# Performance work log

Measured on AMD Instinct MI355X. Metric: run time of the kernel, lower is better.

The kernel has to match this reference:

```python
import jax, jax.numpy as jnp
import numpy as np

D = 256; NH = 8; NL = 4; NP = 4; DFF = 2048; HD = D // NH
SHAPES = [(64, 64), (32, 32), (16, 16), (8, 8)]
B = 2; LEN = sum(h * w for h, w in SHAPES)


def setup_inputs() -> dict:
    key = jax.random.key(0)
    ks = jax.random.split(key, 12)
    def w(k, shape, s=0.02):
        return jax.random.normal(k, shape, jnp.float32) * s
    starts = np.cumsum([0] + [h * w for h, w in SHAPES[:-1]])
    return {
        "src": jax.random.normal(ks[0], (B, LEN, D), jnp.float32),
        "pos": jax.random.normal(ks[1], (B, LEN, D), jnp.float32) * 0.1,
        "spatial_shapes": jnp.array(SHAPES, dtype=jnp.int32),
        "level_start_index": jnp.array(starts, dtype=jnp.int32),
        "w_value": w(ks[2], (D, D)), "b_value": jnp.zeros((D,), jnp.float32),
        "w_off": w(ks[3], (D, NH * NL * NP * 2)), "b_off": w(ks[4], (NH * NL * NP * 2,), 0.1),
        "w_attn": w(ks[5], (D, NH * NL * NP)), "b_attn": jnp.zeros((NH * NL * NP,), jnp.float32),
        "w_out": w(ks[6], (D, D)), "b_out": jnp.zeros((D,), jnp.float32),
        "w1": w(ks[7], (D, DFF)), "b1": jnp.zeros((DFF,), jnp.float32),
        "w2": w(ks[8], (DFF, D)), "b2": jnp.zeros((D,), jnp.float32),
        "g1": jnp.ones((D,), jnp.float32), "be1": jnp.zeros((D,), jnp.float32),
        "g2": jnp.ones((D,), jnp.float32), "be2": jnp.zeros((D,), jnp.float32),
    }


def _layer_norm(x, g, b):
    mu = jnp.mean(x, -1, keepdims=True)
    v = jnp.var(x, -1, keepdims=True)
    return (x - mu) * jax.lax.rsqrt(v + 1e-5) * g + b


def _reference_points(shapes):
    # torch.linspace(0.5, H-0.5, H)/H == (arange(H)+0.5)/H
    refs = []
    for H, W in shapes:
        ry = (jnp.arange(H, dtype=jnp.float32) + 0.5) / H
        rx = (jnp.arange(W, dtype=jnp.float32) + 0.5) / W
        yy, xx = jnp.meshgrid(ry, rx, indexing='ij')
        refs.append(jnp.stack([xx.ravel(), yy.ravel()], -1))
    return jnp.concatenate(refs, 0)  # (Len, 2) as (x, y)


def _ms_deform_sample(value, loc, shapes):
    # value: (B, Len, NH, HD); loc: (B, Lq, NH, NL, NP, 2) normalized [0,1]
    # Replicates torch grid_sample(bilinear, padding='zeros', align_corners=False).
    Bn, Lq = loc.shape[0], loc.shape[1]
    P = loc.shape[4]
    start = 0
    outs = []
    for lvl, (H, W) in enumerate(shapes):
        v = value[:, start:start + H * W].transpose(0, 2, 1, 3)  # (B, NH, HW, HD)
        start += H * W
        l = loc[:, :, :, lvl]                      # (B, Lq, NH, P, 2)
        x = l[..., 0] * W - 0.5
        y = l[..., 1] * H - 0.5
        x0 = jnp.floor(x); y0 = jnp.floor(y)
        dx = x - x0; dy = y - y0
        x0i = x0.astype(jnp.int32); y0i = y0.astype(jnp.int32)
        acc = None
        for xi, yi, wgt in ((x0i, y0i, (1 - dx) * (1 - dy)),
                            (x0i + 1, y0i, dx * (1 - dy)),
                            (x0i, y0i + 1, (1 - dx) * dy),
                            (x0i + 1, y0i + 1, dx * dy)):
            valid = ((xi >= 0) & (xi < W) & (yi >= 0) & (yi < H)).astype(value.dtype)
            idx = jnp.clip(yi, 0, H - 1) * W + jnp.clip(xi, 0, W - 1)  # (B, Lq, NH, P)
            idx = idx.transpose(0, 2, 1, 3).reshape(Bn, NH, Lq * P)
            g = jnp.take_along_axis(v, idx[..., None], axis=2).reshape(Bn, NH, Lq, P, HD)
            w = (wgt * valid).transpose(0, 2, 1, 3)[..., None]  # (B, NH, Lq, P, 1)
            acc = g * w if acc is None else acc + g * w
        outs.append(acc)  # (B, NH, Lq, P, HD)
    return jnp.stack(outs, 3)  # (B, NH, Lq, NL, NP, HD)


def _forward(src, pos, w_value, b_value, w_off, b_off, w_attn, b_attn,
             w_out, b_out, w1, b1, w2, b2, g1, be1, g2, be2, shapes):
    Bn, Lq, _ = src.shape
    q = src + pos  # with_pos_embed
    value = (src @ w_value + b_value).reshape(Bn, Lq, NH, HD)
    off = (q @ w_off + b_off).reshape(Bn, Lq, NH, NL, NP, 2)
    attn = jax.nn.softmax((q @ w_attn + b_attn).reshape(Bn, Lq, NH, NL * NP), -1)
    attn = attn.reshape(Bn, Lq, NH, NL, NP)
    ref = _reference_points(shapes)  # (Len, 2)
    normalizer = jnp.array([[w_, h_] for h_, w_ in shapes], jnp.float32)  # (NL, 2) = (W, H)
    loc = ref[None, :, None, None, None, :] + off / normalizer[None, None, None, :, None, :]
    sampled = _ms_deform_sample(value, loc, shapes)  # (B, NH, Lq, NL, NP, HD)
    out = jnp.einsum('bqhlp,bhqlpd->bqhd', attn, sampled).reshape(Bn, Lq, D)
    out = out @ w_out + b_out
    x = _layer_norm(src + out, g1, be1)           # residual + norm1
    ff = jax.nn.relu(x @ w1 + b1) @ w2 + b2       # FFN (dropout=0)
    return _layer_norm(x + ff, g2, be2)           # residual + norm2


def reference(src, pos, spatial_shapes, level_start_index, w_value, b_value,
              w_off, b_off, w_attn, b_attn, w_out, b_out, w1, b1, w2, b2,
              g1, be1, g2, be2):
    shapes = [tuple(int(v) for v in s) for s in np.asarray(spatial_shapes)]
    return _forward(src, pos, w_value, b_value, w_off, b_off, w_attn, b_attn,
                    w_out, b_out, w1, b1, w2, b2, g1, be1, g2, be2, shapes)
```

## Files before the change

### kernel.cpp

```cpp
#include <hip/hip_runtime.h>
#include <math.h>

#define D 256
#define NH 8
#define NL 4
#define NP 4
#define DFF 2048
#define HD 32
#define BB 2
#define LEN 5440
#define MROWS (BB * LEN)

typedef __attribute__((ext_vector_type(8))) short short8;
typedef __attribute__((ext_vector_type(4))) float f32x4;
typedef unsigned int uint32;

__device__ __forceinline__ unsigned short f2bf(float f) {
    uint32 u = __float_as_uint(f);
    u += 0x7FFF + ((u >> 16) & 1);
    return (unsigned short)(u >> 16);
}
__device__ __forceinline__ float bf2f(unsigned short h) {
    return __uint_as_float(((uint32)h) << 16);
}
__device__ __forceinline__ uint32 pack2(float a, float b) {
    return (uint32)f2bf(a) | ((uint32)f2bf(b) << 16);
}

__device__ __forceinline__ void gl16(const unsigned short* g, unsigned short* l) {
    __builtin_amdgcn_global_load_lds(
        (const __attribute__((address_space(1))) unsigned int*)g,
        (__attribute__((address_space(3))) unsigned int*)l, 16, 0, 0);
}

__device__ __forceinline__ void swz85(int b, int ncols, int& row, int& col) {
    const int gsz = ncols << 3;
    const int full = 10 * gsz;
    if (b < full) {
        const int g = b / gsz, idx = b - g * gsz;
        row = (g << 3) + (idx & 7);
        col = idx >> 3;
    } else {
        const int idx = b - full;
        row = 80 + idx % 5;
        col = idx / 5;
    }
}

__global__ void prep_a(const float* __restrict__ w_value, const float* __restrict__ w_off,
                       const float* __restrict__ w_attn,
                       const float* __restrict__ b_value, const float* __restrict__ b_off,
                       const float* __restrict__ b_attn,
                       const float* __restrict__ src, const float* __restrict__ pos,
                       unsigned short* __restrict__ wqvT, float* __restrict__ bqv,
                       unsigned short* __restrict__ s16, unsigned short* __restrict__ q16) {
    __shared__ float tile[32][33];
    const int blk = blockIdx.x;
    const int t = threadIdx.x;
    if (blk < 160) {
        const float* W; unsigned short* WT; int N, tid;
        if (blk < 64)       { W = w_value; WT = wqvT;             N = 256; tid = blk; }
        else if (blk < 128) { W = w_off;   WT = wqvT + 256 * 256; N = 256; tid = blk - 64; }
        else                { W = w_attn;  WT = wqvT + 512 * 256; N = 128; tid = blk - 128; }
        const int K = 256;
        const int ntx = N >> 5;
        const int nb = (tid % ntx) * 32, kb = (tid / ntx) * 32;
        const int tx = t & 31, ty = t >> 5;
#pragma unroll
        for (int i = 0; i < 32; i += 8)
            tile[ty + i][tx] = W[(size_t)(kb + ty + i) * N + nb + tx];
        __syncthreads();
#pragma unroll
        for (int i = 0; i < 32; i += 8)
            WT[(size_t)(nb + ty + i) * K + kb + tx] = f2bf(tile[tx][ty + i]);
    } else if (blk == 160) {
        for (int i = t; i < 640; i += 256)
            bqv[i] = (i < 256) ? b_value[i] : (i < 512 ? b_off[i - 256] : b_attn[i - 512]);
    } else {
        const int tid = blk - 161;
        const size_t base = (size_t)tid * 4096;
        const float4* s4 = (const float4*)src;
        const float4* p4 = (const float4*)pos;
        ushort4* so = (ushort4*)s16;
        ushort4* qo = (ushort4*)q16;
#pragma unroll
        for (int i = 0; i < 16; i++) {
            const size_t gidx = base + (size_t)i * 256 + t;
            float4 a = s4[gidx], p = p4[gidx];
            ushort4 sv, qv;
            sv.x = f2bf(a.x); sv.y = f2bf(a.y); sv.z = f2bf(a.z); sv.w = f2bf(a.w);
            qv.x = f2bf(a.x + p.x); qv.y = f2bf(a.y + p.y);
            qv.z = f2bf(a.z + p.z); qv.w = f2bf(a.w + p.w);
            so[gidx] = sv; qo[gidx] = qv;
        }
    }
}

__global__ __launch_bounds__(256) void ffn1_gemm(
        const unsigned short* __restrict__ A,
        const unsigned short* __restrict__ BT, const float* __restrict__ bias,
        unsigned short* __restrict__ Cv, int N, int K, int lda, int ldb) {
    __shared__ unsigned short smraw[17408];
    auto Ash = (unsigned short (*)[128][32])smraw;
    auto Bsh = (unsigned short (*)[128][32])(smraw + 8192);

    int rowt, colt;
    swz85(blockIdx.x, N >> 7, rowt, colt);
    const int row0 = rowt * 128, col0 = colt * 128;

    const int t = threadIdx.x;
    const int wave = t >> 6, lane = t & 63;
    const int wr = wave >> 1, wc = wave & 1;
    const int lrow = lane & 15, quad = lane >> 4;
    const int sr = lane >> 2, sc = (lane & 3) * 8;

    const unsigned short* Ab = A + (size_t)row0 * lda;
    const unsigned short* Bb = BT + (size_t)col0 * ldb;

    f32x4 acc[4][4];
#pragma unroll
    for (int i = 0; i < 4; i++)
#pragma unroll
        for (int j = 0; j < 4; j++) acc[i][j] = (f32x4){0.f, 0.f, 0.f, 0.f};

    auto stage = [&](int buf, int kb) {
#pragma unroll
        for (int j = 0; j < 2; j++) {
            const int r = wave * 32 + j * 16;
            gl16(Ab + (size_t)(r + sr) * lda + kb + sc, &Ash[buf][r][0]);
            gl16(Bb + (size_t)(r + sr) * ldb + kb + sc, &Bsh[buf][r][0]);
        }
    };

    stage(0, 0);
    int i = 0;
    for (int kb = 0; kb < K; kb += 32, ++i) {
        __syncthreads();
        if (kb + 32 < K) stage((i + 1) & 1, kb + 32);
        const int cf = i & 1;
        short8 af[4], bfr[4];
#pragma unroll
        for (int mt = 0; mt < 4; mt++)
            af[mt] = *(const short8*)&Ash[cf][wr * 64 + mt * 16 + lrow][quad * 8];
#pragma unroll
        for (int nt = 0; nt < 4; nt++)
            bfr[nt] = *(const short8*)&Bsh[cf][wc * 64 + nt * 16 + lrow][quad * 8];
#pragma unroll
        for (int mt = 0; mt < 4; mt++)
#pragma unroll
            for (int nt = 0; nt < 4; nt++)
                acc[mt][nt] = __builtin_amdgcn_mfma_f32_16x16x32_bf16(
                    af[mt], bfr[nt], acc[mt][nt], 0, 0, 0);
    }

    __syncthreads();
    auto bounce = (unsigned short (*)[136])smraw;
#pragma unroll
    for (int nt = 0; nt < 4; nt++) {
        const int cl = wc * 64 + nt * 16 + lrow;
        const float bv = bias[col0 + cl];
#pragma unroll
        for (int mt = 0; mt < 4; mt++) {
            f32x4 a = acc[mt][nt];
#pragma unroll
            for (int r = 0; r < 4; r++)
                bounce[wr * 64 + mt * 16 + quad * 4 + r][cl] = f2bf(fmaxf(a[r] + bv, 0.f));
        }
    }
    __syncthreads();
#pragma unroll
    for (int pass = 0; pass < 8; pass++) {
        const int rl = pass * 16 + (t >> 4), ch = t & 15;
        *(uint4*)&Cv[(size_t)(row0 + rl) * N + col0 + ch * 8] =
            *(const uint4*)&bounce[rl][ch * 8];
    }
}

template <int NZ>
__global__ __launch_bounds__(256) void splitk_gemm(
        const unsigned short* __restrict__ A, const unsigned short* __restrict__ BT,
        unsigned short* __restrict__ part, int KC, int lda, int ldb) {
    __shared__ unsigned short smraw[17408];
    auto Ash = (unsigned short (*)[128][32])smraw;
    auto Bsh = (unsigned short (*)[128][32])(smraw + 8192);

    int rowt, cc;
    swz85(blockIdx.x, 2 * NZ, rowt, cc);
    const int row0 = rowt * 128;
    const int col0 = (cc & 1) * 128;
    const int z = cc >> 1;
    const int koff = z * KC;
    unsigned short* __restrict__ C = part + (size_t)z * MROWS * 256;

    const int t = threadIdx.x;
    const int wave = t >> 6, lane = t & 63;
    const int wr = wave >> 1, wc = wave & 1;
    const int lrow = lane & 15, quad = lane >> 4;
    const int sr = lane >> 2, sc = (lane & 3) * 8;

    const unsigned short* Ab = A + (size_t)row0 * lda + koff;
    const unsigned short* Bb = BT + (size_t)col0 * ldb + koff;

    f32x4 acc[4][4];
#pragma unroll
    for (int i = 0; i < 4; i++)
#pragma unroll
        for (int j = 0; j < 4; j++) acc[i][j] = (f32x4){0.f, 0.f, 0.f, 0.f};

    auto stage = [&](int buf, int kb) {
#pragma unroll
        for (int j = 0; j < 2; j++) {
            const int r = wave * 32 + j * 16;
            gl16(Ab + (size_t)(r + sr) * lda + kb + sc, &Ash[buf][r][0]);
            gl16(Bb + (size_t)(r + sr) * ldb + kb + sc, &Bsh[buf][r][0]);
        }
    };

    stage(0, 0);
    int i = 0;
    for (int kb = 0; kb < KC; kb += 32, ++i) {
        __syncthreads();
        if (kb + 32 < KC) stage((i + 1) & 1, kb + 32);
        const int cf = i & 1;
        short8 af[4], bfr[4];
#pragma unroll
        for (int mt = 0; mt < 4; mt++)
            af[mt] = *(const short8*)&Ash[cf][wr * 64 + mt * 16 + lrow][quad * 8];
#pragma unroll
        for (int nt = 0; nt < 4; nt++)
            bfr[nt] = *(const short8*)&Bsh[cf][wc * 64 + nt * 16 + lrow][quad * 8];
#pragma unroll
        for (int mt = 0; mt < 4; mt++)
#pragma unroll
            for (int nt = 0; nt < 4; nt++)
                acc[mt][nt] = __builtin_amdgcn_mfma_f32_16x16x32_bf16(
                    af[mt], bfr[nt], acc[mt][nt], 0, 0, 0);
    }

    __syncthreads();
    auto bounce = (unsigned short (*)[136])smraw;
#pragma unroll
    for (int nt = 0; nt < 4; nt++) {
        const int cl = wc * 64 + nt * 16 + lrow;
#pragma unroll
        for (int mt = 0; mt < 4; mt++) {
            f32x4 a = acc[mt][nt];
#pragma unroll
            for (int r = 0; r < 4; r++)
                bounce[wr * 64 + mt * 16 + quad * 4 + r][cl] = f2bf(a[r]);
        }
    }
    __syncthreads();
#pragma unroll
    for (int pass = 0; pass < 8; pass++) {
        const int rl = pass * 16 + (t >> 4), ch = t & 15;
        *(uint4*)&C[(size_t)(row0 + rl) * 256 + col0 + ch * 8] =
            *(const uint4*)&bounce[rl][ch * 8];
    }
}

__global__ __launch_bounds__(256) void gemm_ln(
        const unsigned short* __restrict__ A, const unsigned short* __restrict__ BT,
        const float* __restrict__ bias, const float* __restrict__ rsd,
        const float* __restrict__ g, const float* __restrict__ be,
        unsigned short* __restrict__ out16, int K) {
    __shared__ unsigned short Ash[2][32][32];
    __shared__ unsigned short Bsh[2][256][32];
    __shared__ float red1[4][32], red2[4][32];

    const int row0 = blockIdx.x * 32;
    const int t = threadIdx.x;
    const int wave = t >> 6, lane = t & 63;
    const int lrow = lane & 15, quad = lane >> 4;
    const int sr = lane >> 2, sc = (lane & 3) * 8;

    f32x4 acc[2][4];
#pragma unroll
    for (int i = 0; i < 2; i++)
#pragma unroll
        for (int j = 0; j < 4; j++) acc[i][j] = (f32x4){0.f, 0.f, 0.f, 0.f};

    auto stage = [&](int buf, int kb) {
#pragma unroll
        for (int j = 0; j < 4; j++) {
            const int r = wave * 64 + j * 16;
            gl16(BT + (size_t)(r + sr) * K + kb + sc, &Bsh[buf][r][0]);
        }
        if (wave < 2) {
            const int r = wave * 16;
            gl16(A + (size_t)(row0 + r + sr) * K + kb + sc, &Ash[buf][r][0]);
        }
    };

    stage(0, 0);
    int it = 0;
    for (int kb = 0; kb < K; kb += 32, ++it) {
        __syncthreads();
        if (kb + 32 < K) stage((it + 1) & 1, kb + 32);
        const int cf = it & 1;
        short8 af[2], bfr[4];
#pragma unroll
        for (int mt = 0; mt < 2; mt++)
            af[mt] = *(const short8*)&Ash[cf][mt * 16 + lrow][quad * 8];
#pragma unroll
        for (int nt = 0; nt < 4; nt++)
            bfr[nt] = *(const short8*)&Bsh[cf][wave * 64 + nt * 16 + lrow][quad * 8];
#pragma unroll
        for (int mt = 0; mt < 2; mt++)
#pragma unroll
            for (int nt = 0; nt < 4; nt++)
                acc[mt][nt] = __builtin_amdgcn_mfma_f32_16x16x32_bf16(
                    af[mt], bfr[nt], acc[mt][nt], 0, 0, 0);
    }

    float gv[4], bev[4], bv[4];
#pragma unroll
    for (int nt = 0; nt < 4; nt++) {
        const int col = wave * 64 + nt * 16 + lrow;
        bv[nt] = bias[col];
        gv[nt] = g[col];
        bev[nt] = be[col];
    }

    float v[2][4][4];
#pragma unroll
    for (int mt = 0; mt < 2; mt++)
#pragma unroll
        for (int r = 0; r < 4; r++) {
            const int row = row0 + mt * 16 + quad * 4 + r;
#pragma unroll
            for (int nt = 0; nt < 4; nt++) {
                const int col = wave * 64 + nt * 16 + lrow;
                v[mt][nt][r] = acc[mt][nt][r] + bv[nt] + rsd[(size_t)row * 256 + col];
            }
        }

#pragma unroll
    for (int mt = 0; mt < 2; mt++)
#pragma unroll
        for (int r = 0; r < 4; r++) {
            float s1 = v[mt][0][r] + v[mt][1][r] + v[mt][2][r] + v[mt][3][r];
            float s2 = v[mt][0][r] * v[mt][0][r] + v[mt][1][r] * v[mt][1][r] +
                       v[mt][2][r] * v[mt][2][r] + v[mt][3][r] * v[mt][3][r];
#pragma unroll
            for (int o = 1; o < 16; o <<= 1) {
                s1 += __shfl_xor(s1, o, 16);
                s2 += __shfl_xor(s2, o, 16);
            }
            if (lrow == 0) {
                const int rr = mt * 16 + quad * 4 + r;
                red1[wave][rr] = s1;
                red2[wave][rr] = s2;
            }
        }
    __syncthreads();

#pragma unroll
    for (int mt = 0; mt < 2; mt++)
#pragma unroll
        for (int r = 0; r < 4; r++) {
            const int rr = mt * 16 + quad * 4 + r;
            const float su = red1[0][rr] + red1[1][rr] + red1[2][rr] + red1[3][rr];
            const float sq = red2[0][rr] + red2[1][rr] + red2[2][rr] + red2[3][rr];
            const float mean = su * (1.0f / 256.0f);
            const float var = fmaxf(sq * (1.0f / 256.0f) - mean * mean, 0.f);
            const float rstd = rsqrtf(var + 1e-5f);
            const size_t rowoff = (size_t)(row0 + rr) * 256;
#pragma unroll
            for (int nt = 0; nt < 4; nt++) {
                const int col = wave * 64 + nt * 16 + lrow;
                const float o = (v[mt][nt][r] - mean) * rstd * gv[nt] + bev[nt];
                out16[rowoff + col] = f2bf(o);
            }
        }
}

__global__ __launch_bounds__(256) void qv_gemm(
        const unsigned short* __restrict__ s16, const unsigned short* __restrict__ q16,
        const unsigned short* __restrict__ BT, const float* __restrict__ bias,
        unsigned short* __restrict__ val, unsigned short* __restrict__ qout16) {
    __shared__ unsigned short smraw[17408];
    auto Ash = (unsigned short (*)[128][32])smraw;
    auto Bsh = (unsigned short (*)[128][32])(smraw + 8192);

    int rowt, colt;
    swz85(blockIdx.x, 5, rowt, colt);
    const int row0 = rowt * 128, col0 = colt * 128;

    const int t = threadIdx.x;
    const int wave = t >> 6, lane = t & 63;
    const int wr = wave >> 1, wc = wave & 1;
    const int lrow = lane & 15, quad = lane >> 4;
    const int sr = lane >> 2, sc = (lane & 3) * 8;

    const unsigned short* Ab = ((col0 >= 256) ? q16 : s16) + (size_t)row0 * 256;
    const unsigned short* Bb = BT + (size_t)col0 * 256;

    f32x4 acc[4][4];
#pragma unroll
    for (int i = 0; i < 4; i++)
#pragma unroll
        for (int j = 0; j < 4; j++) acc[i][j] = (f32x4){0.f, 0.f, 0.f, 0.f};

    auto stage = [&](int buf, int kb) {
#pragma unroll
        for (int j = 0; j < 2; j++) {
            const int r = wave * 32 + j * 16;
            gl16(Ab + (size_t)(r + sr) * 256 + kb + sc, &Ash[buf][r][0]);
            gl16(Bb + (size_t)(r + sr) * 256 + kb + sc, &Bsh[buf][r][0]);
        }
    };

    stage(0, 0);
    int i = 0;
    for (int kb = 0; kb < 256; kb += 32, ++i) {
        __syncthreads();
        if (kb + 32 < 256) stage((i + 1) & 1, kb + 32);
        const int cf = i & 1;
        short8 af[4], bfr[4];
#pragma unroll
        for (int mt = 0; mt < 4; mt++)
            af[mt] = *(const short8*)&Ash[cf][wr * 64 + mt * 16 + lrow][quad * 8];
#pragma unroll
        for (int nt = 0; nt < 4; nt++)
            bfr[nt] = *(const short8*)&Bsh[cf][wc * 64 + nt * 16 + lrow][quad * 8];
#pragma unroll
        for (int mt = 0; mt < 4; mt++)
#pragma unroll
            for (int nt = 0; nt < 4; nt++)
                acc[mt][nt] = __builtin_amdgcn_mfma_f32_16x16x32_bf16(
                    af[mt], bfr[nt], acc[mt][nt], 0, 0, 0);
    }

    __syncthreads();
    auto bounce = (unsigned short (*)[136])smraw;
#pragma unroll
    for (int nt = 0; nt < 4; nt++) {
        const int cl = wc * 64 + nt * 16 + lrow;
        const float bv = bias[col0 + cl];
#pragma unroll
        for (int mt = 0; mt < 4; mt++) {
            f32x4 a = acc[mt][nt];
#pragma unroll
            for (int r = 0; r < 4; r++)
                bounce[wr * 64 + mt * 16 + quad * 4 + r][cl] = f2bf(a[r] + bv);
        }
    }
    __syncthreads();
    unsigned short* Cp; int ldc, c0;
    if (col0 < 256) { Cp = val;    ldc = 256; c0 = col0; }
    else            { Cp = qout16; ldc = 384; c0 = col0 - 256; }
#pragma unroll
    for (int pass = 0; pass < 8; pass++) {
        const int rl = pass * 16 + (t >> 4), ch = t & 15;
        *(uint4*)&Cp[(size_t)(row0 + rl) * ldc + c0 + ch * 8] =
            *(const uint4*)&bounce[rl][ch * 8];
    }
}

__global__ void sampler(const unsigned short* __restrict__ val,
                        const unsigned short* __restrict__ qout16,
                        unsigned short* __restrict__ out,
                        const float* __restrict__ w_out, const float* __restrict__ w1,
                        const float* __restrict__ w2,
                        unsigned short* __restrict__ woT, unsigned short* __restrict__ w1T,
                        unsigned short* __restrict__ w2T) {
    __shared__ __align__(16) int   sIdx[2][128][4];
    __shared__ __align__(16) float sW[2][128][4];
    __shared__ float tileT[32][33];
    const int t = threadIdx.x;

    if (blockIdx.x >= MROWS / 2) {
        const int bk = (int)blockIdx.x - MROWS / 2;
        const float* W; unsigned short* WT; int K, N, tid;
        if (bk < 64)       { W = w_out; WT = woT;  K = 256;  N = 256;  tid = bk; }
        else if (bk < 576) { W = w1;    WT = w1T;  K = 256;  N = 2048; tid = bk - 64; }
        else               { W = w2;    WT = w2T;  K = 2048; N = 256;  tid = bk - 576; }
        const int ntx = N >> 5;
        const int nb = (tid % ntx) * 32, kb = (tid / ntx) * 32;
        const int tx = t & 31, ty = t >> 5;
#pragma unroll
        for (int i = 0; i < 32; i += 8)
            tileT[ty + i][tx] = W[(size_t)(kb + ty + i) * N + nb + tx];
        __syncthreads();
#pragma unroll
        for (int i = 0; i < 32; i += 8)
            WT[(size_t)(nb + ty + i) * K + kb + tx] = f2bf(tileT[tx][ty + i]);
        return;
    }

    const int sub = t >> 7;
    const int tt = t & 127;
    const int bq = blockIdx.x * 2 + sub;
    const int b = bq / LEN, q = bq % LEN;

    {
        const int h = tt >> 4, p = tt & 15;
        const int l = p >> 2;

        float refx, refy;
        if (q < 4096) {
            int rq = q >> 6, cq = q & 63;
            refx = (cq + 0.5f) * (1.0f / 64.0f);
            refy = (rq + 0.5f) * (1.0f / 64.0f);
        } else if (q < 5120) {
            int qq = q - 4096;
            int rq = qq >> 5, cq = qq & 31;
            refx = (cq + 0.5f) * (1.0f / 32.0f);
            refy = (rq + 0.5f) * (1.0f / 32.0f);
        } else if (q < 5376) {
            int qq = q - 5120;
            int rq = qq >> 4, cq = qq & 15;
            refx = (cq + 0.5f) * (1.0f / 16.0f);
            refy = (rq + 0.5f) * (1.0f / 16.0f);
        } else {
            int qq = q - 5376;
            int rq = qq >> 3, cq = qq & 7;
            refx = (cq + 0.5f) * (1.0f / 8.0f);
            refy = (rq + 0.5f) * (1.0f / 8.0f);
        }

        float lv = bf2f(qout16[(size_t)bq * 384 + 256 + tt]);
        float mx = lv;
#pragma unroll
        for (int o = 1; o < 16; o <<= 1) mx = fmaxf(mx, __shfl_xor(mx, o, 16));
        float e = expf(lv - mx);
        float s = e;
#pragma unroll
        for (int o = 1; o < 16; o <<= 1) s += __shfl_xor(s, o, 16);
        const float aw = e / s;

        const uint32 opair = *(const uint32*)&qout16[(size_t)bq * 384 + h * 32 + p * 2];
        const float ox = bf2f((unsigned short)opair);
        const float oy = bf2f((unsigned short)(opair >> 16));

        const int LST[4] = {0, 4096, 5120, 5376};
        const int WW = 64 >> l;
        const float rw = 1.0f / (float)WW;

        float x = (refx + ox * rw) * (float)WW - 0.5f;
        float y = (refy + oy * rw) * (float)WW - 0.5f;
        float x0f = floorf(x), y0f = floorf(y);
        float dx = x - x0f, dy = y - y0f;
        int x0 = (int)x0f, y0 = (int)y0f;

        const int base = (b * LEN + LST[l]) * 256 + h * 32;
        int xs[2] = {x0, x0 + 1}, ys[2] = {y0, y0 + 1};
        float wx[2] = {1.f - dx, dx}, wy[2] = {1.f - dy, dy};
        int ic[4]; float wc4[4];
#pragma unroll
        for (int cy = 0; cy < 2; cy++)
#pragma unroll
            for (int cx = 0; cx < 2; cx++) {
                int xi = xs[cx], yi = ys[cy];
                bool vld = (xi >= 0) && (xi < WW) && (yi >= 0) && (yi < WW);
                int xc = min(max(xi, 0), WW - 1);
                int yc = min(max(yi, 0), WW - 1);
                ic[cy * 2 + cx] = base + (yc * WW + xc) * 256;
                wc4[cy * 2 + cx] = vld ? wx[cx] * wy[cy] * aw : 0.f;
            }
        *(int4*)&sIdx[sub][tt][0] = make_int4(ic[0], ic[1], ic[2], ic[3]);
        *(float4*)&sW[sub][tt][0] = make_float4(wc4[0], wc4[1], wc4[2], wc4[3]);
    }
    __syncthreads();

    const int h = tt >> 4, dp = tt & 15;
    const unsigned short* vald = val + 2 * dp;
    float acc0 = 0.f, acc1 = 0.f;
#pragma unroll 4
    for (int p = 0; p < 16; p++) {
        const int r = h * 16 + p;
        int4 iv = *(const int4*)&sIdx[sub][r][0];
        float4 wv = *(const float4*)&sW[sub][r][0];
        uint32 u0 = *(const uint32*)(vald + iv.x);
        uint32 u1 = *(const uint32*)(vald + iv.y);
        uint32 u2 = *(const uint32*)(vald + iv.z);
        uint32 u3 = *(const uint32*)(vald + iv.w);
        acc0 += bf2f((unsigned short)u0) * wv.x + bf2f((unsigned short)u1) * wv.y +
                bf2f((unsigned short)u2) * wv.z + bf2f((unsigned short)u3) * wv.w;
        acc1 += bf2f((unsigned short)(u0 >> 16)) * wv.x + bf2f((unsigned short)(u1 >> 16)) * wv.y +
                bf2f((unsigned short)(u2 >> 16)) * wv.z + bf2f((unsigned short)(u3 >> 16)) * wv.w;
    }
    *(uint32*)&out[(size_t)bq * D + h * HD + 2 * dp] = pack2(acc0, acc1);
}

__global__ void add_ln4(const unsigned short* __restrict__ part16,
                        const float* __restrict__ bias,
                        const unsigned short* __restrict__ rsd16,
                        const float* __restrict__ g, const float* __restrict__ be,
                        float* __restrict__ out) {
    const int wave = threadIdx.x >> 6, lane = threadIdx.x & 63;
    const int row = blockIdx.x * 4 + wave;
    const int c0 = lane * 4;
    const size_t i = (size_t)row * 256 + c0;

    float v[4];
    {
        ushort4 r = *(const ushort4*)&rsd16[i];
        float4 bv = *(const float4*)&bias[c0];
        v[0] = bf2f(r.x) + bv.x; v[1] = bf2f(r.y) + bv.y;
        v[2] = bf2f(r.z) + bv.z; v[3] = bf2f(r.w) + bv.w;
    }
#pragma unroll
    for (int z = 0; z < 4; z++) {
        ushort4 p = *(const ushort4*)&part16[(size_t)z * MROWS * 256 + i];
        v[0] += bf2f(p.x); v[1] += bf2f(p.y); v[2] += bf2f(p.z); v[3] += bf2f(p.w);
    }
    float s1 = v[0] + v[1] + v[2] + v[3];
    float s2 = v[0] * v[0] + v[1] * v[1] + v[2] * v[2] + v[3] * v[3];
#pragma unroll
    for (int o = 32; o > 0; o >>= 1) {
        s1 += __shfl_xor(s1, o, 64);
        s2 += __shfl_xor(s2, o, 64);
    }
    const float mean = s1 * (1.0f / 256.0f);
    const float var = fmaxf(s2 * (1.0f / 256.0f) - mean * mean, 0.f);
    const float rstd = rsqrtf(var + 1e-5f);

    float4 gv = *(const float4*)&g[c0];
    float4 bev = *(const float4*)&be[c0];
    float4 o4;
    o4.x = (v[0] - mean) * rstd * gv.x + bev.x;
    o4.y = (v[1] - mean) * rstd * gv.y + bev.y;
    o4.z = (v[2] - mean) * rstd * gv.z + bev.z;
    o4.w = (v[3] - mean) * rstd * gv.w + bev.w;
    *(float4*)&out[i] = o4;
}

extern "C" void kernel_launch(void* const* d_in, const int* in_sizes, int n_in,
                              void* d_out, int out_size, void* d_ws, size_t ws_size,
                              hipStream_t stream) {
    const float* src     = (const float*)d_in[0];
    const float* pos     = (const float*)d_in[1];
    const float* w_value = (const float*)d_in[4];
    const float* b_value = (const float*)d_in[5];
    const float* w_off   = (const float*)d_in[6];
    const float* b_off   = (const float*)d_in[7];
    const float* w_attn  = (const float*)d_in[8];
    const float* b_attn  = (const float*)d_in[9];
    const float* w_out   = (const float*)d_in[10];
    const float* b_out   = (const float*)d_in[11];
    const float* w1      = (const float*)d_in[12];
    const float* b1      = (const float*)d_in[13];
    const float* w2      = (const float*)d_in[14];
    const float* b2      = (const float*)d_in[15];
    const float* g1      = (const float*)d_in[16];
    const float* be1     = (const float*)d_in[17];
    const float* g2      = (const float*)d_in[18];
    const float* be2     = (const float*)d_in[19];
    float* out = (float*)d_out;

    size_t off = 0;
    auto alloc = [&](size_t bytes) -> char* {
        char* p = (char*)d_ws + off;
        off += (bytes + 255) & ~(size_t)255;
        return p;
    };
    unsigned short* wqvT = (unsigned short*)alloc((size_t)640 * 256 * 2);
    unsigned short* woT  = (unsigned short*)alloc(256 * 256 * 2);
    unsigned short* w1T  = (unsigned short*)alloc((size_t)2048 * 256 * 2);
    unsigned short* w2T  = (unsigned short*)alloc((size_t)256 * 2048 * 2);
    float* bqv           = (float*)alloc(640 * 4);

    unsigned short* s16  = (unsigned short*)alloc((size_t)MROWS * 256 * 2);
    unsigned short* q16  = (unsigned short*)alloc((size_t)MROWS * 256 * 2);
    unsigned short* qout = (unsigned short*)alloc((size_t)MROWS * 384 * 2);
    unsigned short* val  = (unsigned short*)alloc((size_t)MROWS * 256 * 2);
    unsigned short* attn = (unsigned short*)alloc((size_t)MROWS * 256 * 2);
    unsigned short* hb   = (unsigned short*)alloc((size_t)MROWS * 2048 * 2);
    unsigned short* xb16 = (unsigned short*)alloc((size_t)MROWS * 256 * 2);
    unsigned short* part = (unsigned short*)alloc((size_t)4 * MROWS * 256 * 2);

    prep_a<<<331, 256, 0, stream>>>(w_value, w_off, w_attn, b_value, b_off, b_attn,
                                    src, pos, wqvT, bqv, s16, q16);

    qv_gemm<<<425, 256, 0, stream>>>(s16, q16, wqvT, bqv, val, qout);
    sampler<<<MROWS / 2 + 1088, 256, 0, stream>>>(val, qout, attn,
                                                  w_out, w1, w2, woT, w1T, w2T);
    gemm_ln<<<340, 256, 0, stream>>>(attn, woT, b_out, src, g1, be1, xb16, 256);

    ffn1_gemm<<<1360, 256, 0, stream>>>(xb16, w1T, b1, hb, 2048, 256, 256, 256);
    splitk_gemm<4><<<680, 256, 0, stream>>>(hb, w2T, part, 512, 2048, 2048);
    add_ln4<<<MROWS / 4, 256, 0, stream>>>(part, b2, xb16, g2, be2, out);
}
```

Before: 201.7 us.

## Fuse src/pos bf16 conversion into QV GEMM and widen sampler per-thread work

The fp32 to bf16 conversion of src and src+pos moves out of prep_a and into the QV GEMM's A-tile staging. The GEMM now loads fp32 rows with register prefetch one stage ahead, adds pos only for the offset/attention columns, packs to bf16 and writes to a padded LDS tile. This removes the s16/q16 intermediate buffers and their write/read traffic, at the cost of reading fp32 A (twice for q columns) and doing conversion work inside the GEMM. Separately, the sampler now handles four queries per block, with each thread gathering four channels via ushort4 instead of two, which halves the block count and widens each gather.

```diff
diff --git a/kernel.cpp b/kernel.cpp
--- a/kernel.cpp
+++ b/kernel.cpp
@@ -51,49 +51,30 @@
                        const float* __restrict__ w_attn,
                        const float* __restrict__ b_value, const float* __restrict__ b_off,
                        const float* __restrict__ b_attn,
-                       const float* __restrict__ src, const float* __restrict__ pos,
-                       unsigned short* __restrict__ wqvT, float* __restrict__ bqv,
-                       unsigned short* __restrict__ s16, unsigned short* __restrict__ q16) {
+                       unsigned short* __restrict__ wqvT, float* __restrict__ bqv) {
     __shared__ float tile[32][33];
     const int blk = blockIdx.x;
     const int t = threadIdx.x;
-    if (blk < 160) {
-        const float* W; unsigned short* WT; int N, tid;
-        if (blk < 64)       { W = w_value; WT = wqvT;             N = 256; tid = blk; }
-        else if (blk < 128) { W = w_off;   WT = wqvT + 256 * 256; N = 256; tid = blk - 64; }
-        else                { W = w_attn;  WT = wqvT + 512 * 256; N = 128; tid = blk - 128; }
-        const int K = 256;
-        const int ntx = N >> 5;
-        const int nb = (tid % ntx) * 32, kb = (tid / ntx) * 32;
-        const int tx = t & 31, ty = t >> 5;
-#pragma unroll
-        for (int i = 0; i < 32; i += 8)
-            tile[ty + i][tx] = W[(size_t)(kb + ty + i) * N + nb + tx];
-        __syncthreads();
-#pragma unroll
-        for (int i = 0; i < 32; i += 8)
-            WT[(size_t)(nb + ty + i) * K + kb + tx] = f2bf(tile[tx][ty + i]);
-    } else if (blk == 160) {
+    if (blk >= 160) {
         for (int i = t; i < 640; i += 256)
             bqv[i] = (i < 256) ? b_value[i] : (i < 512 ? b_off[i - 256] : b_attn[i - 512]);
-    } else {
-        const int tid = blk - 161;
-        const size_t base = (size_t)tid * 4096;
-        const float4* s4 = (const float4*)src;
-        const float4* p4 = (const float4*)pos;
-        ushort4* so = (ushort4*)s16;
-        ushort4* qo = (ushort4*)q16;
-#pragma unroll
-        for (int i = 0; i < 16; i++) {
-            const size_t gidx = base + (size_t)i * 256 + t;
-            float4 a = s4[gidx], p = p4[gidx];
-            ushort4 sv, qv;
-            sv.x = f2bf(a.x); sv.y = f2bf(a.y); sv.z = f2bf(a.z); sv.w = f2bf(a.w);
-            qv.x = f2bf(a.x + p.x); qv.y = f2bf(a.y + p.y);
-            qv.z = f2bf(a.z + p.z); qv.w = f2bf(a.w + p.w);
-            so[gidx] = sv; qo[gidx] = qv;
-        }
-    }
+        return;
+    }
+    const float* W; unsigned short* WT; int N, tid;
+    if (blk < 64)       { W = w_value; WT = wqvT;             N = 256; tid = blk; }
+    else if (blk < 128) { W = w_off;   WT = wqvT + 256 * 256; N = 256; tid = blk - 64; }
+    else                { W = w_attn;  WT = wqvT + 512 * 256; N = 128; tid = blk - 128; }
+    const int K = 256;
+    const int ntx = N >> 5;
+    const int nb = (tid % ntx) * 32, kb = (tid / ntx) * 32;
+    const int tx = t & 31, ty = t >> 5;
+#pragma unroll
+    for (int i = 0; i < 32; i += 8)
+        tile[ty + i][tx] = W[(size_t)(kb + ty + i) * N + nb + tx];
+    __syncthreads();
+#pragma unroll
+    for (int i = 0; i < 32; i += 8)
+        WT[(size_t)(nb + ty + i) * K + kb + tx] = f2bf(tile[tx][ty + i]);
 }
 
 __global__ __launch_bounds__(256) void ffn1_gemm(
@@ -376,24 +357,28 @@
 }
 
 __global__ __launch_bounds__(256) void qv_gemm(
-        const unsigned short* __restrict__ s16, const unsigned short* __restrict__ q16,
+        const float* __restrict__ src, const float* __restrict__ pos,
         const unsigned short* __restrict__ BT, const float* __restrict__ bias,
         unsigned short* __restrict__ val, unsigned short* __restrict__ qout16) {
-    __shared__ unsigned short smraw[17408];
-    auto Ash = (unsigned short (*)[128][32])smraw;
-    auto Bsh = (unsigned short (*)[128][32])(smraw + 8192);
+    __shared__ unsigned short smraw[18432];
+    auto Ash = (unsigned short (*)[128][40])smraw;
+    auto Bsh = (unsigned short (*)[128][32])(smraw + 10240);
 
     int rowt, colt;
     swz85(blockIdx.x, 5, rowt, colt);
     const int row0 = rowt * 128, col0 = colt * 128;
+    const bool addp = (col0 >= 256);
 
     const int t = threadIdx.x;
     const int wave = t >> 6, lane = t & 63;
     const int wr = wave >> 1, wc = wave & 1;
     const int lrow = lane & 15, quad = lane >> 4;
+    const int srow = t >> 1;
+    const int cb = (t & 1) * 16;
     const int sr = lane >> 2, sc = (lane & 3) * 8;
 
-    const unsigned short* Ab = ((col0 >= 256) ? q16 : s16) + (size_t)row0 * 256;
+    const float* ap = src + (size_t)(row0 + srow) * 256 + cb;
+    const float* pp = pos + (size_t)(row0 + srow) * 256 + cb;
     const unsigned short* Bb = BT + (size_t)col0 * 256;
 
     f32x4 acc[4][4];
@@ -402,20 +387,51 @@
 #pragma unroll
         for (int j = 0; j < 4; j++) acc[i][j] = (f32x4){0.f, 0.f, 0.f, 0.f};
 
-    auto stage = [&](int buf, int kb) {
+    float4 fa[4]; float4 fp[4];
+    auto packA = [&](int buf) {
+        float4 f0 = fa[0], f1 = fa[1], f2 = fa[2], f3 = fa[3];
+        if (addp) {
+            f0.x += fp[0].x; f0.y += fp[0].y; f0.z += fp[0].z; f0.w += fp[0].w;
+            f1.x += fp[1].x; f1.y += fp[1].y; f1.z += fp[1].z; f1.w += fp[1].w;
+            f2.x += fp[2].x; f2.y += fp[2].y; f2.z += fp[2].z; f2.w += fp[2].w;
+            f3.x += fp[3].x; f3.y += fp[3].y; f3.z += fp[3].z; f3.w += fp[3].w;
+        }
+        uint4 u0 = make_uint4(pack2(f0.x, f0.y), pack2(f0.z, f0.w),
+                              pack2(f1.x, f1.y), pack2(f1.z, f1.w));
+        uint4 u1 = make_uint4(pack2(f2.x, f2.y), pack2(f2.z, f2.w),
+                              pack2(f3.x, f3.y), pack2(f3.z, f3.w));
+        *(uint4*)&Ash[buf][srow][cb + 0] = u0;
+        *(uint4*)&Ash[buf][srow][cb + 8] = u1;
+    };
+    auto loadA = [&](int kb) {
+#pragma unroll
+        for (int j = 0; j < 4; j++) fa[j] = *(const float4*)(ap + kb + 4 * j);
+        if (addp) {
+#pragma unroll
+            for (int j = 0; j < 4; j++) fp[j] = *(const float4*)(pp + kb + 4 * j);
+        }
+    };
+    auto stageB = [&](int buf, int kb) {
 #pragma unroll
         for (int j = 0; j < 2; j++) {
             const int r = wave * 32 + j * 16;
-            gl16(Ab + (size_t)(r + sr) * 256 + kb + sc, &Ash[buf][r][0]);
             gl16(Bb + (size_t)(r + sr) * 256 + kb + sc, &Bsh[buf][r][0]);
         }
     };
 
-    stage(0, 0);
+    loadA(0);
+    packA(0);
+    stageB(0, 0);
+    loadA(32);
+
     int i = 0;
     for (int kb = 0; kb < 256; kb += 32, ++i) {
         __syncthreads();
-        if (kb + 32 < 256) stage((i + 1) & 1, kb + 32);
+        if (kb + 32 < 256) {
+            stageB((i + 1) & 1, kb + 32);
+            packA((i + 1) & 1);
+            if (kb + 64 < 256) loadA(kb + 64);
+        }
         const int cf = i & 1;
         short8 af[4], bfr[4];
 #pragma unroll
@@ -465,13 +481,13 @@
                         const float* __restrict__ w2,
                         unsigned short* __restrict__ woT, unsigned short* __restrict__ w1T,
                         unsigned short* __restrict__ w2T) {
-    __shared__ __align__(16) int   sIdx[2][128][4];
-    __shared__ __align__(16) float sW[2][128][4];
+    __shared__ __align__(16) int   sIdx[4][128][4];
+    __shared__ __align__(16) float sW[4][128][4];
     __shared__ float tileT[32][33];
     const int t = threadIdx.x;
 
-    if (blockIdx.x >= MROWS / 2) {
-        const int bk = (int)blockIdx.x - MROWS / 2;
+    if (blockIdx.x >= MROWS / 4) {
+        const int bk = (int)blockIdx.x - MROWS / 4;
         const float* W; unsigned short* WT; int K, N, tid;
         if (bk < 64)       { W = w_out; WT = woT;  K = 256;  N = 256;  tid = bk; }
         else if (bk < 576) { W = w1;    WT = w1T;  K = 256;  N = 2048; tid = bk - 64; }
@@ -489,14 +505,16 @@
         return;
     }
 
-    const int sub = t >> 7;
-    const int tt = t & 127;
-    const int bq = blockIdx.x * 2 + sub;
-    const int b = bq / LEN, q = bq % LEN;
-
-    {
-        const int h = tt >> 4, p = tt & 15;
-        const int l = p >> 2;
+    const int pair = t & 127;
+    const int qsel = t >> 7;
+    const int h1 = pair >> 4, p1 = pair & 15;
+    const int lvl = p1 >> 2;
+
+#pragma unroll
+    for (int j = 0; j < 2; j++) {
+        const int ql = qsel + 2 * j;
+        const int bq = (int)blockIdx.x * 4 + ql;
+        const int b = bq / LEN, q = bq % LEN;
 
         float refx, refy;
         if (q < 4096) {
@@ -520,7 +538,7 @@
             refy = (rq + 0.5f) * (1.0f / 8.0f);
         }
 
-        float lv = bf2f(qout16[(size_t)bq * 384 + 256 + tt]);
+        float lv = bf2f(qout16[(size_t)bq * 384 + 256 + pair]);
         float mx = lv;
 #pragma unroll
         for (int o = 1; o < 16; o <<= 1) mx = fmaxf(mx, __shfl_xor(mx, o, 16));
@@ -530,12 +548,12 @@
         for (int o = 1; o < 16; o <<= 1) s += __shfl_xor(s, o, 16);
         const float aw = e / s;
 
-        const uint32 opair = *(const uint32*)&qout16[(size_t)bq * 384 + h * 32 + p * 2];
+        const uint32 opair = *(const uint32*)&qout16[(size_t)bq * 384 + h1 * 32 + p1 * 2];
         const float ox = bf2f((unsigned short)opair);
         const float oy = bf2f((unsigned short)(opair >> 16));
 
         const int LST[4] = {0, 4096, 5120, 5376};
-        const int WW = 64 >> l;
+        const int WW = 64 >> lvl;
         const float rw = 1.0f / (float)WW;
 
         float x = (refx + ox * rw) * (float)WW - 0.5f;
@@ -544,7 +562,7 @@
         float dx = x - x0f, dy = y - y0f;
         int x0 = (int)x0f, y0 = (int)y0f;
 
-        const int base = (b * LEN + LST[l]) * 256 + h * 32;
+        const int base = (b * LEN + LST[lvl]) * 256 + h1 * 32;
         int xs[2] = {x0, x0 + 1}, ys[2] = {y0, y0 + 1};
         float wx[2] = {1.f - dx, dx}, wy[2] = {1.f - dy, dy};
         int ic[4]; float wc4[4];
@@ -559,29 +577,36 @@
                 ic[cy * 2 + cx] = base + (yc * WW + xc) * 256;
                 wc4[cy * 2 + cx] = vld ? wx[cx] * wy[cy] * aw : 0.f;
             }
-        *(int4*)&sIdx[sub][tt][0] = make_int4(ic[0], ic[1], ic[2], ic[3]);
-        *(float4*)&sW[sub][tt][0] = make_float4(wc4[0], wc4[1], wc4[2], wc4[3]);
-    }
-    __syncthreads();
-
-    const int h = tt >> 4, dp = tt & 15;
-    const unsigned short* vald = val + 2 * dp;
-    float acc0 = 0.f, acc1 = 0.f;
+        *(int4*)&sIdx[ql][pair][0] = make_int4(ic[0], ic[1], ic[2], ic[3]);
+        *(float4*)&sW[ql][pair][0] = make_float4(wc4[0], wc4[1], wc4[2], wc4[3]);
+    }
+    __syncthreads();
+
+    const int g = t >> 6;
+    const int l6 = t & 63;
+    const int h = l6 >> 3;
+    const int c4 = (l6 & 7) * 4;
+    const int bq = (int)blockIdx.x * 4 + g;
+    const unsigned short* vald = val + c4;
+    float a0 = 0.f, a1 = 0.f, a2 = 0.f, a3 = 0.f;
 #pragma unroll 4
     for (int p = 0; p < 16; p++) {
         const int r = h * 16 + p;
-        int4 iv = *(const int4*)&sIdx[sub][r][0];
-        float4 wv = *(const float4*)&sW[sub][r][0];
-        uint32 u0 = *(const uint32*)(vald + iv.x);
-        uint32 u1 = *(const uint32*)(vald + iv.y);
-        uint32 u2 = *(const uint32*)(vald + iv.z);
-        uint32 u3 = *(const uint32*)(vald + iv.w);
-        acc0 += bf2f((unsigned short)u0) * wv.x + bf2f((unsigned short)u1) * wv.y +
-                bf2f((unsigned short)u2) * wv.z + bf2f((unsigned short)u3) * wv.w;
-        acc1 += bf2f((unsigned short)(u0 >> 16)) * wv.x + bf2f((unsigned short)(u1 >> 16)) * wv.y +
-                bf2f((unsigned short)(u2 >> 16)) * wv.z + bf2f((unsigned short)(u3 >> 16)) * wv.w;
-    }
-    *(uint32*)&out[(size_t)bq * D + h * HD + 2 * dp] = pack2(acc0, acc1);
+        int4 iv = *(const int4*)&sIdx[g][r][0];
+        float4 wv = *(const float4*)&sW[g][r][0];
+        ushort4 u0 = *(const ushort4*)(vald + iv.x);
+        ushort4 u1 = *(const ushort4*)(vald + iv.y);
+        ushort4 u2 = *(const ushort4*)(vald + iv.z);
+        ushort4 u3 = *(const ushort4*)(vald + iv.w);
+        a0 += bf2f(u0.x) * wv.x + bf2f(u1.x) * wv.y + bf2f(u2.x) * wv.z + bf2f(u3.x) * wv.w;
+        a1 += bf2f(u0.y) * wv.x + bf2f(u1.y) * wv.y + bf2f(u2.y) * wv.z + bf2f(u3.y) * wv.w;
+        a2 += bf2f(u0.z) * wv.x + bf2f(u1.z) * wv.y + bf2f(u2.z) * wv.z + bf2f(u3.z) * wv.w;
+        a3 += bf2f(u0.w) * wv.x + bf2f(u1.w) * wv.y + bf2f(u2.w) * wv.z + bf2f(u3.w) * wv.w;
+    }
+    uint2 o2;
+    o2.x = pack2(a0, a1);
+    o2.y = pack2(a2, a3);
+    *(uint2*)&out[(size_t)bq * D + h * HD + c4] = o2;
 }
 
 __global__ void add_ln4(const unsigned short* __restrict__ part16,
@@ -662,8 +687,6 @@
     unsigned short* w2T  = (unsigned short*)alloc((size_t)256 * 2048 * 2);
     float* bqv           = (float*)alloc(640 * 4);
 
-    unsigned short* s16  = (unsigned short*)alloc((size_t)MROWS * 256 * 2);
-    unsigned short* q16  = (unsigned short*)alloc((size_t)MROWS * 256 * 2);
     unsigned short* qout = (unsigned short*)alloc((size_t)MROWS * 384 * 2);
     unsigned short* val  = (unsigned short*)alloc((size_t)MROWS * 256 * 2);
     unsigned short* attn = (unsigned short*)alloc((size_t)MROWS * 256 * 2);
@@ -671,11 +694,11 @@
     unsigned short* xb16 = (unsigned short*)alloc((size_t)MROWS * 256 * 2);
     unsigned short* part = (unsigned short*)alloc((size_t)4 * MROWS * 256 * 2);
 
-    prep_a<<<331, 256, 0, stream>>>(w_value, w_off, w_attn, b_value, b_off, b_attn,
-                                    src, pos, wqvT, bqv, s16, q16);
-
-    qv_gemm<<<425, 256, 0, stream>>>(s16, q16, wqvT, bqv, val, qout);
-    sampler<<<MROWS / 2 + 1088, 256, 0, stream>>>(val, qout, attn,
+    prep_a<<<161, 256, 0, stream>>>(w_value, w_off, w_attn, b_value, b_off, b_attn,
+                                    wqvT, bqv);
+
+    qv_gemm<<<425, 256, 0, stream>>>(src, pos, wqvT, bqv, val, qout);
+    sampler<<<MROWS / 4 + 1088, 256, 0, stream>>>(val, qout, attn,
                                                   w_out, w1, w2, woT, w1T, w2T);
     gemm_ln<<<340, 256, 0, stream>>>(attn, woT, b_out, src, g1, be1, xb16, 256);
 
```

Measured after the change: 204.2 us. Within noise of the previous version (+1.2%).
